# Performance work log

Hardware: AMD Instinct MI355X
Metric: run time of the kernel (lower is better)

Reference implementation:

```python
import jax, jax.numpy as jnp
import numpy as np

D_MODEL = 1024
N_HEADS = 16
D_HEAD = D_MODEL // N_HEADS
BLOCK = 128
B, T = 2, 2048


def setup_inputs() -> dict:
    key = jax.random.key(0)
    ks = jax.random.split(key, 5)
    x = jax.random.normal(ks[0], (B, T, D_MODEL), dtype=jnp.float32)
    def init_w(k):
        # nn.Linear default init scale ~ 1/sqrt(fan_in)
        return jax.random.normal(k, (D_MODEL, D_MODEL), dtype=jnp.float32) / np.sqrt(D_MODEL).astype(np.float32)
    return {
        "x": x,
        "Wq": init_w(ks[1]),
        "Wk": init_w(ks[2]),
        "Wv": init_w(ks[3]),
        "Wo": init_w(ks[4]),
    }


def _flash_attention(Q, K, V, block_size, scale):
    """Online-softmax tiled attention over kv blocks (causal). Q,K,V: (B,H,T,d)."""
    Bb, H, Tt, d = Q.shape
    n_blocks = Tt // block_size
    # (n_blocks, B, H, block, d) so scan streams kv tiles
    Kb = K.reshape(Bb, H, n_blocks, block_size, d).transpose(2, 0, 1, 3, 4)
    Vb = V.reshape(Bb, H, n_blocks, block_size, d).transpose(2, 0, 1, 3, 4)
    starts = jnp.arange(n_blocks) * block_size
    q_pos = jnp.arange(Tt)

    def step(carry, xs):
        m, l, acc = carry
        kb, vb, st = xs
        # scores: (B,H,T,block)
        scores = scale * jnp.einsum('bhtd,bhsd->bhts', Q, kb)
        kv_pos = st + jnp.arange(block_size)
        future = kv_pos[None, :] > q_pos[:, None]          # (T, block)
        scores = jnp.where(future[None, None], -jnp.inf, scores)
        m_new = jnp.maximum(m, jnp.max(scores, axis=-1, keepdims=True))
        p = jnp.exp(scores - m_new)
        corr = jnp.exp(m - m_new)
        l = corr * l + jnp.sum(p, axis=-1, keepdims=True)
        acc = corr * acc + jnp.einsum('bhts,bhsd->bhtd', p, vb)
        return (m_new, l, acc), None

    m0 = jnp.full((Bb, H, Tt, 1), -jnp.inf, dtype=jnp.float32)
    l0 = jnp.zeros((Bb, H, Tt, 1), dtype=jnp.float32)
    a0 = jnp.zeros((Bb, H, Tt, d), dtype=jnp.float32)
    (m, l, acc), _ = jax.lax.scan(step, (m0, l0, a0), (Kb, Vb, starts))
    return acc / jnp.maximum(l, 1e-12)


def reference(x, Wq, Wk, Wv, Wo):
    Bx, Tx, _ = x.shape
    scale = 1.0 / np.sqrt(D_HEAD).astype(np.float32)
    def proj(W):  # nn.Linear: y = x @ W.T
        y = jnp.einsum('btm,nm->btn', x, W)
        return y.reshape(Bx, Tx, N_HEADS, D_HEAD).transpose(0, 2, 1, 3)
    Q, K, V = proj(Wq), proj(Wk), proj(Wv)
    O = _flash_attention(Q.astype(jnp.float32), K.astype(jnp.float32), V.astype(jnp.float32), BLOCK, scale)
    O = O.astype(x.dtype).transpose(0, 2, 1, 3).reshape(Bx, Tx, D_MODEL)
    return jnp.einsum('btm,nm->btn', O, Wo)
```

## Files before the change

### kernel.cpp

```cpp
#include <hip/hip_runtime.h>
#include <hip/hip_bf16.h>

typedef __attribute__((ext_vector_type(8))) short short8;
typedef __attribute__((ext_vector_type(4))) float f32x4;
typedef __attribute__((ext_vector_type(2))) unsigned int uint2v;
typedef __attribute__((ext_vector_type(4))) unsigned int uint4v;
typedef unsigned short u16;

#define MFMA_BF16(a, b, c) __builtin_amdgcn_mfma_f32_16x16x32_bf16(a, b, c, 0, 0, 0)

#define T_SEQ 2048
#define DMODEL 1024
#define NHEADS 16
#define DHEAD 64
#define NEG_BIG (-30000.0f)
#define QSCALE 0.1803368801111f
#define RESCALE_THR 8.0f

#if __has_builtin(__builtin_amdgcn_exp2f)
#define EXP2(x) __builtin_amdgcn_exp2f(x)
#else
#define EXP2(x) exp2f(x)
#endif

__device__ __forceinline__ unsigned bfr(unsigned u) {
  return (u + 0x7fffu + ((u >> 16) & 1u)) >> 16;
}
__device__ __forceinline__ uint4v ld8bf(const float* __restrict__ p) {
  const uint4v a = *(const uint4v*)p;
  const uint4v b = *(const uint4v*)(p + 4);
  uint4v r;
  r[0] = bfr(a[0]) | (bfr(a[1]) << 16);
  r[1] = bfr(a[2]) | (bfr(a[3]) << 16);
  r[2] = bfr(b[0]) | (bfr(b[1]) << 16);
  r[3] = bfr(b[2]) | (bfr(b[3]) << 16);
  return r;
}
__device__ __forceinline__ u16 f2bf(float f) {
  unsigned u = __float_as_uint(f);
  u += 0x7fffu + ((u >> 16) & 1u);
  return (u16)(u >> 16);
}
__device__ __forceinline__ void gld16(const u16* g, u16* l) {
  __builtin_amdgcn_global_load_lds(
      (const __attribute__((address_space(1))) unsigned int*)g,
      (__attribute__((address_space(3))) unsigned int*)l, 16, 0, 0);
}

__global__ __launch_bounds__(256) void cvt_all(
    const float* __restrict__ x, const float* __restrict__ wq,
    const float* __restrict__ wk, const float* __restrict__ wv,
    const float* __restrict__ wo, u16* __restrict__ xh, u16* __restrict__ wqh,
    u16* __restrict__ wkh, u16* __restrict__ wvh, u16* __restrict__ woh) {
  int bi = blockIdx.x;
  const float* s;
  u16* d;
  size_t base;
  if (bi < 2048) {
    s = x; d = xh; base = (size_t)bi * 2048;
  } else {
    int k = (bi - 2048) >> 9;
    int r = (bi - 2048) & 511;
    s = (k == 0) ? wq : (k == 1) ? wk : (k == 2) ? wv : wo;
    d = (k == 0) ? wqh : (k == 1) ? wkh : (k == 2) ? wvh : woh;
    base = (size_t)r * 2048;
  }
  size_t i = base + (size_t)threadIdx.x * 8;
  *(uint4v*)&d[i] = ld8bf(&s[i]);
}

__global__ __launch_bounds__(256) void gemm_qkv(
    const u16* __restrict__ X, const u16* __restrict__ Wq,
    const u16* __restrict__ Wk, const u16* __restrict__ Wv,
    u16* __restrict__ Qo, u16* __restrict__ Ko, u16* __restrict__ Vo) {
  __shared__ __attribute__((aligned(16))) u16 As[2][128 * 32];
  __shared__ __attribute__((aligned(16))) u16 Bs[2][128 * 32];
  const int tid = threadIdx.x, lane = tid & 63, w = tid >> 6;
  const int wm = (w >> 1) * 64, wn = (w & 1) * 64;
  const int lrow = lane & 15;
  const int lk = (lane >> 4) << 3;
  const int lq = (lane >> 4) << 2;
  const int mBase = blockIdx.x * 128, nBase = blockIdx.y * 128;
  const u16* Bt = (blockIdx.z == 0) ? Wq : (blockIdx.z == 1) ? Wk : Wv;
  u16* D = (blockIdx.z == 0) ? Qo : (blockIdx.z == 1) ? Ko : Vo;
  const float scale = (blockIdx.z == 0) ? QSCALE : 1.0f;

  f32x4 acc[4][4];
#pragma unroll
  for (int mi = 0; mi < 4; mi++)
#pragma unroll
    for (int ni = 0; ni < 4; ni++) acc[mi][ni] = (f32x4)0.0f;

  auto stage = [&](int buf, int k0) {
#pragma unroll
    for (int i = 0; i < 2; i++) {
      int c = i * 256 + tid;
      int r = c >> 2, kk = (c & 3) << 3;
      gld16(&X[(size_t)(mBase + r) * 1024 + k0 + kk], &As[buf][c * 8]);
      gld16(&Bt[(size_t)(nBase + r) * 1024 + k0 + kk], &Bs[buf][c * 8]);
    }
  };

  stage(0, 0);
  __syncthreads();
  int cur = 0;
  for (int k0 = 0; k0 < 1024; k0 += 32) {
    if (k0 + 32 < 1024) stage(cur ^ 1, k0 + 32);
    short8 af[4], bf[4];
#pragma unroll
    for (int mi = 0; mi < 4; mi++)
      af[mi] = *(const short8*)&As[cur][(wm + mi * 16 + lrow) * 32 + lk];
#pragma unroll
    for (int ni = 0; ni < 4; ni++)
      bf[ni] = *(const short8*)&Bs[cur][(wn + ni * 16 + lrow) * 32 + lk];
#pragma unroll
    for (int mi = 0; mi < 4; mi++)
#pragma unroll
      for (int ni = 0; ni < 4; ni++)
        acc[mi][ni] = MFMA_BF16(af[mi], bf[ni], acc[mi][ni]);
    __syncthreads();
    cur ^= 1;
  }
  const int vz = (blockIdx.z == 2);
#pragma unroll
  for (int mi = 0; mi < 4; mi++)
#pragma unroll
    for (int r = 0; r < 4; r++) {
      int m = mBase + wm + mi * 16 + lq + r;
      int b = m >> 11, t = m & 2047;
#pragma unroll
      for (int ni = 0; ni < 4; ni++) {
        int n = nBase + wn + ni * 16 + lrow;
        int h = n >> 6, dd = n & 63;
        size_t idx = vz ? (((size_t)((b * NHEADS + h) * DHEAD + dd)) * T_SEQ + t)
                        : ((((size_t)(b * NHEADS + h)) * T_SEQ + t) * DHEAD + dd);
        D[idx] = f2bf(acc[mi][ni][r] * scale);
      }
    }
}

__global__ __launch_bounds__(256) void attn_snake(
    const u16* __restrict__ Qg, const u16* __restrict__ Kg,
    const u16* __restrict__ Vtg, u16* __restrict__ Ob) {
  __shared__ __attribute__((aligned(16))) u16 smem[20992];
  u16* Qs = smem;
  u16* Ps = smem;

  const int tid = threadIdx.x;
  const int w = tid >> 6, lane = tid & 63;
  const int lrow = lane & 15;
  const int quad = lane >> 4;
  const int lk = quad << 3;
  const int rsw = lrow & 7;
  const int q_local = w * 16 + lrow;

  const int id = blockIdx.x;
  const int j = (id >> 3) & 15;
  const int bh = (id & 7) * 4 + ((id >> 7) & 3);
  const int b = bh >> 4, h = bh & 15;
  const u16* Qp = Qg + (size_t)bh * T_SEQ * DHEAD;
  const u16* Kp = Kg + (size_t)bh * T_SEQ * DHEAD;
  const u16* Vp = Vtg + (size_t)bh * DHEAD * T_SEQ;

  auto stage_kv = [&](u16* Ksd, u16* Vtd, int kvb) {
#pragma unroll
    for (int i = 0; i < 2; i++) {
      int c = i * 256 + tid;
      int r = c >> 3;
      int sw = ((c & 7) ^ (r & 7)) << 3;
      gld16(&Kp[(size_t)(kvb + r) * DHEAD + sw], &Ksd[c * 8]);
      gld16(&Vp[(size_t)r * T_SEQ + kvb + sw], &Vtd[c * 8]);
    }
  };

#pragma unroll
  for (int p = 0; p < 2; p++) {
    const int qt = p ? (31 - j) : j;
    const int qb = qt * 64;

    __syncthreads();
#pragma unroll
    for (int i = 0; i < 2; i++) {
      int c = i * 256 + tid;
      int r = c >> 3, kk = (c & 7) << 3;
      *(uint4v*)&Qs[r * 72 + kk] =
          *(const uint4v*)&Qp[(size_t)(qb + r) * DHEAD + kk];
    }
    stage_kv(smem + 4608, smem + 12800, 0);
    __syncthreads();

    short8 qf[2];
#pragma unroll
    for (int ks = 0; ks < 2; ks++)
      qf[ks] = *(const short8*)&Qs[q_local * 72 + ks * 32 + lk];

    float mst = NEG_BIG, lst = 0.f;
    f32x4 oacc[4];
#pragma unroll
    for (int nd = 0; nd < 4; nd++) oacc[nd] = (f32x4)0.0f;

    const int ntiles = qt + 1;
    int cur = 0;
    for (int kt = 0; kt < ntiles; kt++) {
      u16* Ksc = smem + 4608 + cur * 4096;
      u16* Vtc = smem + 12800 + cur * 4096;
      if (kt + 1 < ntiles)
        stage_kv(smem + 4608 + (cur ^ 1) * 4096,
                 smem + 12800 + (cur ^ 1) * 4096, (kt + 1) * 64);

      f32x4 s[4];
      __builtin_amdgcn_s_setprio(1);
#pragma unroll
      for (int kvt = 0; kvt < 4; kvt++) {
        f32x4 a = (f32x4)0.0f;
#pragma unroll
        for (int ks = 0; ks < 2; ks++) {
          short8 kf = *(const short8*)&Ksc[(kvt * 16 + lrow) * 64 +
                                           ((((ks << 2) + quad) ^ rsw) << 3)];
          a = MFMA_BF16(kf, qf[ks], a);
        }
        s[kvt] = a;
      }
      __builtin_amdgcn_s_setprio(0);

      if (kt == qt) {
#pragma unroll
        for (int kvt = 0; kvt < 4; kvt++)
#pragma unroll
          for (int r = 0; r < 4; r++)
            if (kvt * 16 + quad * 4 + r > q_local) s[kvt][r] = NEG_BIG;
      }

      float mx = s[0][0];
#pragma unroll
      for (int kvt = 0; kvt < 4; kvt++)
#pragma unroll
        for (int r = 0; r < 4; r++) mx = fmaxf(mx, s[kvt][r]);
      mx = fmaxf(mx, __shfl_xor(mx, 16));
      mx = fmaxf(mx, __shfl_xor(mx, 32));
      if (!__all(mx <= mst + RESCALE_THR)) {
        float mn = fmaxf(mst, mx);
        float corr = EXP2(mst - mn);
        mst = mn;
        lst *= corr;
#pragma unroll
        for (int nd = 0; nd < 4; nd++) oacc[nd] *= corr;
      }
      float ls = 0.f;
#pragma unroll
      for (int kvt = 0; kvt < 4; kvt++)
#pragma unroll
        for (int r = 0; r < 4; r++) {
          float pv = EXP2(s[kvt][r] - mst);
          s[kvt][r] = pv;
          ls += pv;
        }
      ls += __shfl_xor(ls, 16);
      ls += __shfl_xor(ls, 32);
      lst += ls;

#pragma unroll
      for (int kvt = 0; kvt < 4; kvt++) {
        uint2v pk;
        pk[0] = (__float_as_uint(s[kvt][0]) >> 16) |
                (__float_as_uint(s[kvt][1]) & 0xffff0000u);
        pk[1] = (__float_as_uint(s[kvt][2]) >> 16) |
                (__float_as_uint(s[kvt][3]) & 0xffff0000u);
        *(uint2v*)&Ps[q_local * 72 + kvt * 16 + quad * 4] = pk;
      }

      __builtin_amdgcn_s_setprio(1);
#pragma unroll
      for (int ks = 0; ks < 2; ks++) {
        short8 pf = *(const short8*)&Ps[q_local * 72 + ks * 32 + lk];
#pragma unroll
        for (int nd = 0; nd < 4; nd++) {
          short8 vf = *(const short8*)&Vtc[(nd * 16 + lrow) * 64 +
                                           ((((ks << 2) + quad) ^ rsw) << 3)];
          oacc[nd] = MFMA_BF16(vf, pf, oacc[nd]);
        }
      }
      __builtin_amdgcn_s_setprio(0);

      __syncthreads();
      cur ^= 1;
    }

    float inv = 1.f / lst;
    size_t rowbase = ((size_t)(b * T_SEQ + qb + q_local)) * DMODEL + h * DHEAD;
#pragma unroll
    for (int nd = 0; nd < 4; nd++) {
      uint2v pk;
      pk[0] = (unsigned)f2bf(oacc[nd][0] * inv) |
              ((unsigned)f2bf(oacc[nd][1] * inv) << 16);
      pk[1] = (unsigned)f2bf(oacc[nd][2] * inv) |
              ((unsigned)f2bf(oacc[nd][3] * inv) << 16);
      *(uint2v*)&Ob[rowbase + nd * 16 + quad * 4] = pk;
    }
  }
}

__global__ __launch_bounds__(256) void gemm_out_bf(const u16* __restrict__ O,
                                                   const u16* __restrict__ Wo,
                                                   float* __restrict__ Out) {
  __shared__ __attribute__((aligned(16))) u16 As[2][128 * 32];
  __shared__ __attribute__((aligned(16))) u16 Bs[2][64 * 32];
  const int tid = threadIdx.x, lane = tid & 63, w = tid >> 6;
  const int wm = (w >> 1) * 64, wn = (w & 1) * 32;
  const int lrow = lane & 15;
  const int lk = (lane >> 4) << 3;
  const int lq = (lane >> 4) << 2;
  const int mBase = blockIdx.x * 128, nBase = blockIdx.y * 64;

  f32x4 acc[4][2];
#pragma unroll
  for (int mi = 0; mi < 4; mi++)
#pragma unroll
    for (int ni = 0; ni < 2; ni++) acc[mi][ni] = (f32x4)0.0f;

  auto stage = [&](int buf, int k0) {
#pragma unroll
    for (int i = 0; i < 2; i++) {
      int c = i * 256 + tid;
      int r = c >> 2, kk = (c & 3) << 3;
      gld16(&O[(size_t)(mBase + r) * 1024 + k0 + kk], &As[buf][c * 8]);
    }
    int r = tid >> 2, kk = (tid & 3) << 3;
    gld16(&Wo[(size_t)(nBase + r) * 1024 + k0 + kk], &Bs[buf][tid * 8]);
  };

  stage(0, 0);
  __syncthreads();
  int cur = 0;
  for (int k0 = 0; k0 < 1024; k0 += 32) {
    if (k0 + 32 < 1024) stage(cur ^ 1, k0 + 32);
    short8 af[4], bf[2];
#pragma unroll
    for (int mi = 0; mi < 4; mi++)
      af[mi] = *(const short8*)&As[cur][(wm + mi * 16 + lrow) * 32 + lk];
#pragma unroll
    for (int ni = 0; ni < 2; ni++)
      bf[ni] = *(const short8*)&Bs[cur][(wn + ni * 16 + lrow) * 32 + lk];
#pragma unroll
    for (int mi = 0; mi < 4; mi++)
#pragma unroll
      for (int ni = 0; ni < 2; ni++)
        acc[mi][ni] = MFMA_BF16(af[mi], bf[ni], acc[mi][ni]);
    __syncthreads();
    cur ^= 1;
  }
#pragma unroll
  for (int mi = 0; mi < 4; mi++)
#pragma unroll
    for (int r = 0; r < 4; r++) {
      int m = mBase + wm + mi * 16 + lq + r;
#pragma unroll
      for (int ni = 0; ni < 2; ni++)
        Out[(size_t)m * DMODEL + nBase + wn + ni * 16 + lrow] = acc[mi][ni][r];
    }
}

extern "C" void kernel_launch(void* const* d_in, const int* in_sizes, int n_in,
                              void* d_out, int out_size, void* d_ws,
                              size_t ws_size, hipStream_t stream) {
  const float* x = (const float*)d_in[0];
  const float* Wq = (const float*)d_in[1];
  const float* Wk = (const float*)d_in[2];
  const float* Wv = (const float*)d_in[3];
  const float* Wo = (const float*)d_in[4];
  float* out = (float*)d_out;

  u16* xh = (u16*)d_ws;
  u16* wqh = xh + 4194304;
  u16* wkh = wqh + 1048576;
  u16* wvh = wkh + 1048576;
  u16* woh = wvh + 1048576;
  u16* Q = woh + 1048576;
  u16* K = Q + 4194304;
  u16* V = K + 4194304;
  u16* O = V + 4194304;

  cvt_all<<<dim3(4096), 256, 0, stream>>>(x, Wq, Wk, Wv, Wo, xh, wqh, wkh, wvh, woh);
  gemm_qkv<<<dim3(32, 8, 3), 256, 0, stream>>>(xh, wqh, wkh, wvh, Q, K, V);
  attn_snake<<<dim3(512), 256, 0, stream>>>(Q, K, V, O);
  gemm_out_bf<<<dim3(32, 16), 256, 0, stream>>>(O, woh, out);
}
```

Before: 188.2 us.

## Widen attention KV tiles to 128 keys and load Q fragments directly from global

The attention kernel now streams K/V in 128-key tiles instead of 64, halving the number of loop iterations, online-softmax max/sum updates and block barriers per query tile. Q fragments are read straight from global memory into registers instead of staging through shared memory, and the P buffer gains an XOR-swizzled 128-wide layout. The wider tile doubles LDS use (about 80 KB), which may cut occupancy and raise register pressure. Odd query tiles also compute a masked half tile on the diagonal.

```diff
diff --git a/kernel.cpp b/kernel.cpp
--- a/kernel.cpp
+++ b/kernel.cpp
@@ -142,9 +142,7 @@
 __global__ __launch_bounds__(256) void attn_snake(
     const u16* __restrict__ Qg, const u16* __restrict__ Kg,
     const u16* __restrict__ Vtg, u16* __restrict__ Ob) {
-  __shared__ __attribute__((aligned(16))) u16 smem[20992];
-  u16* Qs = smem;
-  u16* Ps = smem;
+  __shared__ __attribute__((aligned(16))) u16 smem[40960];
 
   const int tid = threadIdx.x;
   const int w = tid >> 6, lane = tid & 63;
@@ -162,14 +160,16 @@
   const u16* Kp = Kg + (size_t)bh * T_SEQ * DHEAD;
   const u16* Vp = Vtg + (size_t)bh * DHEAD * T_SEQ;
 
-  auto stage_kv = [&](u16* Ksd, u16* Vtd, int kvb) {
-#pragma unroll
-    for (int i = 0; i < 2; i++) {
+  auto stage_kv = [&](int buf, int kvb) {
+#pragma unroll
+    for (int i = 0; i < 4; i++) {
       int c = i * 256 + tid;
-      int r = c >> 3;
-      int sw = ((c & 7) ^ (r & 7)) << 3;
-      gld16(&Kp[(size_t)(kvb + r) * DHEAD + sw], &Ksd[c * 8]);
-      gld16(&Vp[(size_t)r * T_SEQ + kvb + sw], &Vtd[c * 8]);
+      int rk = c >> 3, gk = c & 7;
+      gld16(&Kp[(size_t)(kvb + rk) * DHEAD + ((gk ^ (rk & 7)) << 3)],
+            &smem[8192 + buf * 8192 + c * 8]);
+      int rv = c >> 4, gv = c & 15;
+      gld16(&Vp[(size_t)rv * T_SEQ + kvb + ((gv ^ (rv & 7)) << 3)],
+            &smem[24576 + buf * 8192 + c * 8]);
     }
   };
 
@@ -177,65 +177,57 @@
   for (int p = 0; p < 2; p++) {
     const int qt = p ? (31 - j) : j;
     const int qb = qt * 64;
+    const int ktd = qt >> 1;
+    const int diagoff = ((qt & 1) << 6) + q_local;
 
     __syncthreads();
-#pragma unroll
-    for (int i = 0; i < 2; i++) {
-      int c = i * 256 + tid;
-      int r = c >> 3, kk = (c & 7) << 3;
-      *(uint4v*)&Qs[r * 72 + kk] =
-          *(const uint4v*)&Qp[(size_t)(qb + r) * DHEAD + kk];
-    }
-    stage_kv(smem + 4608, smem + 12800, 0);
-    __syncthreads();
-
+    stage_kv(0, 0);
     short8 qf[2];
 #pragma unroll
     for (int ks = 0; ks < 2; ks++)
-      qf[ks] = *(const short8*)&Qs[q_local * 72 + ks * 32 + lk];
+      qf[ks] =
+          *(const short8*)&Qp[(size_t)(qb + q_local) * DHEAD + ks * 32 + lk];
 
     float mst = NEG_BIG, lst = 0.f;
     f32x4 oacc[4];
 #pragma unroll
     for (int nd = 0; nd < 4; nd++) oacc[nd] = (f32x4)0.0f;
-
-    const int ntiles = qt + 1;
+    __syncthreads();
+
     int cur = 0;
-    for (int kt = 0; kt < ntiles; kt++) {
-      u16* Ksc = smem + 4608 + cur * 4096;
-      u16* Vtc = smem + 12800 + cur * 4096;
-      if (kt + 1 < ntiles)
-        stage_kv(smem + 4608 + (cur ^ 1) * 4096,
-                 smem + 12800 + (cur ^ 1) * 4096, (kt + 1) * 64);
-
-      f32x4 s[4];
+    for (int kt = 0; kt <= ktd; kt++) {
+      if (kt < ktd) stage_kv(cur ^ 1, (kt + 1) * 128);
+      const u16* Kc = &smem[8192 + cur * 8192];
+      const u16* Vc = &smem[24576 + cur * 8192];
+
+      f32x4 s[8];
       __builtin_amdgcn_s_setprio(1);
 #pragma unroll
-      for (int kvt = 0; kvt < 4; kvt++) {
+      for (int kvt = 0; kvt < 8; kvt++) {
         f32x4 a = (f32x4)0.0f;
 #pragma unroll
         for (int ks = 0; ks < 2; ks++) {
-          short8 kf = *(const short8*)&Ksc[(kvt * 16 + lrow) * 64 +
-                                           ((((ks << 2) + quad) ^ rsw) << 3)];
+          short8 kf = *(const short8*)&Kc[(kvt * 16 + lrow) * 64 +
+                                          ((((ks << 2) + quad) ^ rsw) << 3)];
           a = MFMA_BF16(kf, qf[ks], a);
         }
         s[kvt] = a;
       }
       __builtin_amdgcn_s_setprio(0);
 
-      if (kt == qt) {
-#pragma unroll
-        for (int kvt = 0; kvt < 4; kvt++)
+      if (kt == ktd) {
+#pragma unroll
+        for (int kvt = 0; kvt < 8; kvt++)
 #pragma unroll
           for (int r = 0; r < 4; r++)
-            if (kvt * 16 + quad * 4 + r > q_local) s[kvt][r] = NEG_BIG;
-      }
-
-      float mx = s[0][0];
-#pragma unroll
-      for (int kvt = 0; kvt < 4; kvt++)
-#pragma unroll
-        for (int r = 0; r < 4; r++) mx = fmaxf(mx, s[kvt][r]);
+            if (kvt * 16 + quad * 4 + r > diagoff) s[kvt][r] = NEG_BIG;
+      }
+
+      float mx = NEG_BIG;
+#pragma unroll
+      for (int kvt = 0; kvt < 8; kvt++)
+        mx = fmaxf(mx, fmaxf(fmaxf(s[kvt][0], s[kvt][1]),
+                             fmaxf(s[kvt][2], s[kvt][3])));
       mx = fmaxf(mx, __shfl_xor(mx, 16));
       mx = fmaxf(mx, __shfl_xor(mx, 32));
       if (!__all(mx <= mst + RESCALE_THR)) {
@@ -246,37 +238,43 @@
 #pragma unroll
         for (int nd = 0; nd < 4; nd++) oacc[nd] *= corr;
       }
-      float ls = 0.f;
-#pragma unroll
-      for (int kvt = 0; kvt < 4; kvt++)
-#pragma unroll
-        for (int r = 0; r < 4; r++) {
-          float pv = EXP2(s[kvt][r] - mst);
-          s[kvt][r] = pv;
-          ls += pv;
-        }
+      float e[8];
+#pragma unroll
+      for (int kvt = 0; kvt < 8; kvt++) {
+        f32x4 pv;
+        pv[0] = EXP2(s[kvt][0] - mst);
+        pv[1] = EXP2(s[kvt][1] - mst);
+        pv[2] = EXP2(s[kvt][2] - mst);
+        pv[3] = EXP2(s[kvt][3] - mst);
+        s[kvt] = pv;
+        e[kvt] = (pv[0] + pv[1]) + (pv[2] + pv[3]);
+      }
+      float ls = ((e[0] + e[1]) + (e[2] + e[3])) + ((e[4] + e[5]) + (e[6] + e[7]));
       ls += __shfl_xor(ls, 16);
       ls += __shfl_xor(ls, 32);
       lst += ls;
 
 #pragma unroll
-      for (int kvt = 0; kvt < 4; kvt++) {
+      for (int kvt = 0; kvt < 8; kvt++) {
         uint2v pk;
         pk[0] = (__float_as_uint(s[kvt][0]) >> 16) |
                 (__float_as_uint(s[kvt][1]) & 0xffff0000u);
         pk[1] = (__float_as_uint(s[kvt][2]) >> 16) |
                 (__float_as_uint(s[kvt][3]) & 0xffff0000u);
-        *(uint2v*)&Ps[q_local * 72 + kvt * 16 + quad * 4] = pk;
+        *(uint2v*)&smem[q_local * 128 +
+                        ((((kvt << 1) + (quad >> 1)) ^ rsw) << 3) +
+                        ((quad & 1) << 2)] = pk;
       }
 
       __builtin_amdgcn_s_setprio(1);
 #pragma unroll
-      for (int ks = 0; ks < 2; ks++) {
-        short8 pf = *(const short8*)&Ps[q_local * 72 + ks * 32 + lk];
+      for (int ks = 0; ks < 4; ks++) {
+        short8 pf = *(const short8*)&smem[q_local * 128 +
+                                          ((((ks << 2) + quad) ^ rsw) << 3)];
 #pragma unroll
         for (int nd = 0; nd < 4; nd++) {
-          short8 vf = *(const short8*)&Vtc[(nd * 16 + lrow) * 64 +
-                                           ((((ks << 2) + quad) ^ rsw) << 3)];
+          short8 vf = *(const short8*)&Vc[(nd * 16 + lrow) * 128 +
+                                          ((((ks << 2) + quad) ^ rsw) << 3)];
           oacc[nd] = MFMA_BF16(vf, pf, oacc[nd]);
         }
       }
```

Result: no change. 189.2 us (+0.6%).

## Split attention into one block per query tile and transpose V via LDS

Applied to the files above, without the earlier changes.

The attention kernel now launches one block per 64-row query tile (1024 blocks) instead of pairing tiles in a snake order within a block. Tiles are ordered longest-first and mapped to XCDs so each XCD shares K/V for its heads. Q and P now use an XOR-swizzled unpadded LDS layout, which trims shared memory. The QKV GEMM writes transposed V through an LDS staging tile so the global stores are coalesced 16-byte writes instead of scattered 2-byte ones. The cost is more blocks with their own Q loads and prologue, and load balance now depends on scheduler order.

```diff
diff --git a/kernel.cpp b/kernel.cpp
--- a/kernel.cpp
+++ b/kernel.cpp
@@ -73,8 +73,7 @@
     const u16* __restrict__ X, const u16* __restrict__ Wq,
     const u16* __restrict__ Wk, const u16* __restrict__ Wv,
     u16* __restrict__ Qo, u16* __restrict__ Ko, u16* __restrict__ Vo) {
-  __shared__ __attribute__((aligned(16))) u16 As[2][128 * 32];
-  __shared__ __attribute__((aligned(16))) u16 Bs[2][128 * 32];
+  __shared__ __attribute__((aligned(16))) u16 sm[16384];
   const int tid = threadIdx.x, lane = tid & 63, w = tid >> 6;
   const int wm = (w >> 1) * 64, wn = (w & 1) * 64;
   const int lrow = lane & 15;
@@ -96,8 +95,9 @@
     for (int i = 0; i < 2; i++) {
       int c = i * 256 + tid;
       int r = c >> 2, kk = (c & 3) << 3;
-      gld16(&X[(size_t)(mBase + r) * 1024 + k0 + kk], &As[buf][c * 8]);
-      gld16(&Bt[(size_t)(nBase + r) * 1024 + k0 + kk], &Bs[buf][c * 8]);
+      gld16(&X[(size_t)(mBase + r) * 1024 + k0 + kk], &sm[buf * 4096 + c * 8]);
+      gld16(&Bt[(size_t)(nBase + r) * 1024 + k0 + kk],
+            &sm[8192 + buf * 4096 + c * 8]);
     }
   };
 
@@ -109,10 +109,11 @@
     short8 af[4], bf[4];
 #pragma unroll
     for (int mi = 0; mi < 4; mi++)
-      af[mi] = *(const short8*)&As[cur][(wm + mi * 16 + lrow) * 32 + lk];
+      af[mi] = *(const short8*)&sm[cur * 4096 + (wm + mi * 16 + lrow) * 32 + lk];
 #pragma unroll
     for (int ni = 0; ni < 4; ni++)
-      bf[ni] = *(const short8*)&Bs[cur][(wn + ni * 16 + lrow) * 32 + lk];
+      bf[ni] =
+          *(const short8*)&sm[8192 + cur * 4096 + (wn + ni * 16 + lrow) * 32 + lk];
 #pragma unroll
     for (int mi = 0; mi < 4; mi++)
 #pragma unroll
@@ -121,30 +122,55 @@
     __syncthreads();
     cur ^= 1;
   }
-  const int vz = (blockIdx.z == 2);
-#pragma unroll
-  for (int mi = 0; mi < 4; mi++)
-#pragma unroll
-    for (int r = 0; r < 4; r++) {
-      int m = mBase + wm + mi * 16 + lq + r;
-      int b = m >> 11, t = m & 2047;
-#pragma unroll
-      for (int ni = 0; ni < 4; ni++) {
-        int n = nBase + wn + ni * 16 + lrow;
-        int h = n >> 6, dd = n & 63;
-        size_t idx = vz ? (((size_t)((b * NHEADS + h) * DHEAD + dd)) * T_SEQ + t)
-                        : ((((size_t)(b * NHEADS + h)) * T_SEQ + t) * DHEAD + dd);
-        D[idx] = f2bf(acc[mi][ni][r] * scale);
+
+  if (blockIdx.z != 2) {
+#pragma unroll
+    for (int mi = 0; mi < 4; mi++)
+#pragma unroll
+      for (int r = 0; r < 4; r++) {
+        int m = mBase + wm + mi * 16 + lq + r;
+        int b = m >> 11, t = m & 2047;
+#pragma unroll
+        for (int ni = 0; ni < 4; ni++) {
+          int n = nBase + wn + ni * 16 + lrow;
+          int h = n >> 6, dd = n & 63;
+          D[(((size_t)(b * NHEADS + h)) * T_SEQ + t) * DHEAD + dd] =
+              f2bf(acc[mi][ni][r] * scale);
+        }
       }
-    }
-}
-
-__global__ __launch_bounds__(256) void attn_snake(
+  } else {
+    u16* TT = &sm[w * 4096];
+#pragma unroll
+    for (int mi = 0; mi < 4; mi++)
+#pragma unroll
+      for (int r = 0; r < 4; r++) {
+        int t_loc = mi * 16 + lq + r;
+#pragma unroll
+        for (int ni = 0; ni < 4; ni++) {
+          int d_loc = ni * 16 + lrow;
+          TT[d_loc * 64 + ((((t_loc >> 3) ^ (d_loc & 7)) << 3) | (t_loc & 7))] =
+              f2bf(acc[mi][ni][r]);
+        }
+      }
+    const int b = (mBase + wm) >> 11;
+    const int t0 = (mBase + wm) & 2047;
+#pragma unroll
+    for (int it = 0; it < 8; it++) {
+      int d_loc = it * 8 + (lane >> 3);
+      int ch = lane & 7;
+      short8 v = *(const short8*)&TT[d_loc * 64 + ((ch ^ (d_loc & 7)) << 3)];
+      int n = nBase + wn + d_loc;
+      int h = n >> 6, dd = n & 63;
+      *(uint4v*)&D[(((size_t)((b * NHEADS + h) * DHEAD + dd)) * T_SEQ) + t0 +
+                   ch * 8] = *(const uint4v*)&v;
+    }
+  }
+}
+
+__global__ __launch_bounds__(256) void attn_qt(
     const u16* __restrict__ Qg, const u16* __restrict__ Kg,
     const u16* __restrict__ Vtg, u16* __restrict__ Ob) {
-  __shared__ __attribute__((aligned(16))) u16 smem[20992];
-  u16* Qs = smem;
-  u16* Ps = smem;
+  __shared__ __attribute__((aligned(16))) u16 smem[20480];
 
   const int tid = threadIdx.x;
   const int w = tid >> 6, lane = tid & 63;
@@ -155,148 +181,147 @@
   const int q_local = w * 16 + lrow;
 
   const int id = blockIdx.x;
-  const int j = (id >> 3) & 15;
-  const int bh = (id & 7) * 4 + ((id >> 7) & 3);
+  const int xcd = id & 7;
+  const int r0 = id >> 3;
+  const int rr = r0 & 31;
+  const int bsub = r0 >> 5;
+  const int qt = (bsub & 1) ? rr : (31 - rr);
+  const int bh = xcd * 4 + bsub;
   const int b = bh >> 4, h = bh & 15;
+  const int qb = qt * 64;
   const u16* Qp = Qg + (size_t)bh * T_SEQ * DHEAD;
   const u16* Kp = Kg + (size_t)bh * T_SEQ * DHEAD;
   const u16* Vp = Vtg + (size_t)bh * DHEAD * T_SEQ;
 
-  auto stage_kv = [&](u16* Ksd, u16* Vtd, int kvb) {
+  auto stage_kv = [&](int buf, int kvb) {
 #pragma unroll
     for (int i = 0; i < 2; i++) {
       int c = i * 256 + tid;
       int r = c >> 3;
       int sw = ((c & 7) ^ (r & 7)) << 3;
-      gld16(&Kp[(size_t)(kvb + r) * DHEAD + sw], &Ksd[c * 8]);
-      gld16(&Vp[(size_t)r * T_SEQ + kvb + sw], &Vtd[c * 8]);
+      gld16(&Kp[(size_t)(kvb + r) * DHEAD + sw], &smem[4096 + buf * 4096 + c * 8]);
+      gld16(&Vp[(size_t)r * T_SEQ + kvb + sw], &smem[12288 + buf * 4096 + c * 8]);
     }
   };
 
 #pragma unroll
-  for (int p = 0; p < 2; p++) {
-    const int qt = p ? (31 - j) : j;
-    const int qb = qt * 64;
+  for (int i = 0; i < 2; i++) {
+    int c = i * 256 + tid;
+    int r = c >> 3, g = c & 7;
+    *(uint4v*)&smem[r * 64 + ((g ^ (r & 7)) << 3)] =
+        *(const uint4v*)&Qp[(size_t)(qb + r) * DHEAD + (g << 3)];
+  }
+  stage_kv(0, 0);
+  __syncthreads();
+
+  short8 qf[2];
+#pragma unroll
+  for (int ks = 0; ks < 2; ks++)
+    qf[ks] = *(const short8*)&smem[q_local * 64 + ((((ks << 2) + quad) ^ rsw) << 3)];
+
+  float mst = NEG_BIG, lst = 0.f;
+  f32x4 oacc[4];
+#pragma unroll
+  for (int nd = 0; nd < 4; nd++) oacc[nd] = (f32x4)0.0f;
+
+  const int ntiles = qt + 1;
+  int cur = 0;
+  for (int kt = 0; kt < ntiles; kt++) {
+    const u16* Kc = &smem[4096 + cur * 4096];
+    const u16* Vc = &smem[12288 + cur * 4096];
+    if (kt + 1 < ntiles) stage_kv(cur ^ 1, (kt + 1) * 64);
+
+    f32x4 s[4];
+    __builtin_amdgcn_s_setprio(1);
+#pragma unroll
+    for (int kvt = 0; kvt < 4; kvt++) {
+      f32x4 a = (f32x4)0.0f;
+#pragma unroll
+      for (int ks = 0; ks < 2; ks++) {
+        short8 kf = *(const short8*)&Kc[(kvt * 16 + lrow) * 64 +
+                                        ((((ks << 2) + quad) ^ rsw) << 3)];
+        a = MFMA_BF16(kf, qf[ks], a);
+      }
+      s[kvt] = a;
+    }
+    __builtin_amdgcn_s_setprio(0);
+
+    if (kt == qt) {
+#pragma unroll
+      for (int kvt = 0; kvt < 4; kvt++)
+#pragma unroll
+        for (int r = 0; r < 4; r++)
+          if (kvt * 16 + quad * 4 + r > q_local) s[kvt][r] = NEG_BIG;
+    }
+
+    float mx = NEG_BIG;
+#pragma unroll
+    for (int kvt = 0; kvt < 4; kvt++)
+      mx = fmaxf(mx, fmaxf(fmaxf(s[kvt][0], s[kvt][1]),
+                           fmaxf(s[kvt][2], s[kvt][3])));
+    mx = fmaxf(mx, __shfl_xor(mx, 16));
+    mx = fmaxf(mx, __shfl_xor(mx, 32));
+    if (!__all(mx <= mst + RESCALE_THR)) {
+      float mn = fmaxf(mst, mx);
+      float corr = EXP2(mst - mn);
+      mst = mn;
+      lst *= corr;
+#pragma unroll
+      for (int nd = 0; nd < 4; nd++) oacc[nd] *= corr;
+    }
+    float ls = 0.f;
+#pragma unroll
+    for (int kvt = 0; kvt < 4; kvt++)
+#pragma unroll
+      for (int r = 0; r < 4; r++) {
+        float pv = EXP2(s[kvt][r] - mst);
+        s[kvt][r] = pv;
+        ls += pv;
+      }
+    ls += __shfl_xor(ls, 16);
+    ls += __shfl_xor(ls, 32);
+    lst += ls;
+
+#pragma unroll
+    for (int kvt = 0; kvt < 4; kvt++) {
+      uint2v pk;
+      pk[0] = (__float_as_uint(s[kvt][0]) >> 16) |
+              (__float_as_uint(s[kvt][1]) & 0xffff0000u);
+      pk[1] = (__float_as_uint(s[kvt][2]) >> 16) |
+              (__float_as_uint(s[kvt][3]) & 0xffff0000u);
+      *(uint2v*)&smem[q_local * 64 +
+                      ((((kvt << 1) | (quad >> 1)) ^ rsw) << 3) +
+                      ((quad & 1) << 2)] = pk;
+    }
+
+    __builtin_amdgcn_s_setprio(1);
+#pragma unroll
+    for (int ks = 0; ks < 2; ks++) {
+      short8 pf = *(const short8*)&smem[q_local * 64 +
+                                        ((((ks << 2) + quad) ^ rsw) << 3)];
+#pragma unroll
+      for (int nd = 0; nd < 4; nd++) {
+        short8 vf = *(const short8*)&Vc[(nd * 16 + lrow) * 64 +
+                                        ((((ks << 2) + quad) ^ rsw) << 3)];
+        oacc[nd] = MFMA_BF16(vf, pf, oacc[nd]);
+      }
+    }
+    __builtin_amdgcn_s_setprio(0);
 
     __syncthreads();
-#pragma unroll
-    for (int i = 0; i < 2; i++) {
-      int c = i * 256 + tid;
-      int r = c >> 3, kk = (c & 7) << 3;
-      *(uint4v*)&Qs[r * 72 + kk] =
-          *(const uint4v*)&Qp[(size_t)(qb + r) * DHEAD + kk];
-    }
-    stage_kv(smem + 4608, smem + 12800, 0);
-    __syncthreads();
-
-    short8 qf[2];
-#pragma unroll
-    for (int ks = 0; ks < 2; ks++)
-      qf[ks] = *(const short8*)&Qs[q_local * 72 + ks * 32 + lk];
-
-    float mst = NEG_BIG, lst = 0.f;
-    f32x4 oacc[4];
-#pragma unroll
-    for (int nd = 0; nd < 4; nd++) oacc[nd] = (f32x4)0.0f;
-
-    const int ntiles = qt + 1;
-    int cur = 0;
-    for (int kt = 0; kt < ntiles; kt++) {
-      u16* Ksc = smem + 4608 + cur * 4096;
-      u16* Vtc = smem + 12800 + cur * 4096;
-      if (kt + 1 < ntiles)
-        stage_kv(smem + 4608 + (cur ^ 1) * 4096,
-                 smem + 12800 + (cur ^ 1) * 4096, (kt + 1) * 64);
-
-      f32x4 s[4];
-      __builtin_amdgcn_s_setprio(1);
-#pragma unroll
-      for (int kvt = 0; kvt < 4; kvt++) {
-        f32x4 a = (f32x4)0.0f;
-#pragma unroll
-        for (int ks = 0; ks < 2; ks++) {
-          short8 kf = *(const short8*)&Ksc[(kvt * 16 + lrow) * 64 +
-                                           ((((ks << 2) + quad) ^ rsw) << 3)];
-          a = MFMA_BF16(kf, qf[ks], a);
-        }
-        s[kvt] = a;
-      }
-      __builtin_amdgcn_s_setprio(0);
-
-      if (kt == qt) {
-#pragma unroll
-        for (int kvt = 0; kvt < 4; kvt++)
-#pragma unroll
-          for (int r = 0; r < 4; r++)
-            if (kvt * 16 + quad * 4 + r > q_local) s[kvt][r] = NEG_BIG;
-      }
-
-      float mx = s[0][0];
-#pragma unroll
-      for (int kvt = 0; kvt < 4; kvt++)
-#pragma unroll
-        for (int r = 0; r < 4; r++) mx = fmaxf(mx, s[kvt][r]);
-      mx = fmaxf(mx, __shfl_xor(mx, 16));
-      mx = fmaxf(mx, __shfl_xor(mx, 32));
-      if (!__all(mx <= mst + RESCALE_THR)) {
-        float mn = fmaxf(mst, mx);
-        float corr = EXP2(mst - mn);
-        mst = mn;
-        lst *= corr;
-#pragma unroll
-        for (int nd = 0; nd < 4; nd++) oacc[nd] *= corr;
-      }
-      float ls = 0.f;
-#pragma unroll
-      for (int kvt = 0; kvt < 4; kvt++)
-#pragma unroll
-        for (int r = 0; r < 4; r++) {
-          float pv = EXP2(s[kvt][r] - mst);
-          s[kvt][r] = pv;
-          ls += pv;
-        }
-      ls += __shfl_xor(ls, 16);
-      ls += __shfl_xor(ls, 32);
-      lst += ls;
-
-#pragma unroll
-      for (int kvt = 0; kvt < 4; kvt++) {
-        uint2v pk;
-        pk[0] = (__float_as_uint(s[kvt][0]) >> 16) |
-                (__float_as_uint(s[kvt][1]) & 0xffff0000u);
-        pk[1] = (__float_as_uint(s[kvt][2]) >> 16) |
-                (__float_as_uint(s[kvt][3]) & 0xffff0000u);
-        *(uint2v*)&Ps[q_local * 72 + kvt * 16 + quad * 4] = pk;
-      }
-
-      __builtin_amdgcn_s_setprio(1);
-#pragma unroll
-      for (int ks = 0; ks < 2; ks++) {
-        short8 pf = *(const short8*)&Ps[q_local * 72 + ks * 32 + lk];
-#pragma unroll
-        for (int nd = 0; nd < 4; nd++) {
-          short8 vf = *(const short8*)&Vtc[(nd * 16 + lrow) * 64 +
-                                           ((((ks << 2) + quad) ^ rsw) << 3)];
-          oacc[nd] = MFMA_BF16(vf, pf, oacc[nd]);
-        }
-      }
-      __builtin_amdgcn_s_setprio(0);
-
-      __syncthreads();
-      cur ^= 1;
-    }
-
-    float inv = 1.f / lst;
-    size_t rowbase = ((size_t)(b * T_SEQ + qb + q_local)) * DMODEL + h * DHEAD;
-#pragma unroll
-    for (int nd = 0; nd < 4; nd++) {
-      uint2v pk;
-      pk[0] = (unsigned)f2bf(oacc[nd][0] * inv) |
-              ((unsigned)f2bf(oacc[nd][1] * inv) << 16);
-      pk[1] = (unsigned)f2bf(oacc[nd][2] * inv) |
-              ((unsigned)f2bf(oacc[nd][3] * inv) << 16);
-      *(uint2v*)&Ob[rowbase + nd * 16 + quad * 4] = pk;
-    }
+    cur ^= 1;
+  }
+
+  float inv = 1.f / lst;
+  size_t rowbase = ((size_t)(b * T_SEQ + qb + q_local)) * DMODEL + h * DHEAD;
+#pragma unroll
+  for (int nd = 0; nd < 4; nd++) {
+    uint2v pk;
+    pk[0] = (unsigned)f2bf(oacc[nd][0] * inv) |
+            ((unsigned)f2bf(oacc[nd][1] * inv) << 16);
+    pk[1] = (unsigned)f2bf(oacc[nd][2] * inv) |
+            ((unsigned)f2bf(oacc[nd][3] * inv) << 16);
+    *(uint2v*)&Ob[rowbase + nd * 16 + quad * 4] = pk;
   }
 }
 
@@ -382,6 +407,6 @@
 
   cvt_all<<<dim3(4096), 256, 0, stream>>>(x, Wq, Wk, Wv, Wo, xh, wqh, wkh, wvh, woh);
   gemm_qkv<<<dim3(32, 8, 3), 256, 0, stream>>>(xh, wqh, wkh, wvh, Q, K, V);
-  attn_snake<<<dim3(512), 256, 0, stream>>>(Q, K, V, O);
+  attn_qt<<<dim3(1024), 256, 0, stream>>>(Q, K, V, O);
   gemm_out_bf<<<dim3(32, 16), 256, 0, stream>>>(O, woh, out);
 }
```

Result: faster. 178.2 us (-5.3%).
